# Kernel tuning notes

Measured on AMD Instinct MI355X. Metric: run time of the kernel, lower is better.

Reference implementation:

```python
import jax, jax.numpy as jnp
import numpy as np


def setup_inputs() -> dict:
    key = jax.random.key(0)
    k1, k2 = jax.random.split(key)
    N_ACTIVE = 262144
    C = 64            # nPlanes
    S = 64            # spatial_size per dim (3D)
    B = 8             # batch size
    features = jax.random.normal(k1, (N_ACTIVE, C), dtype=jnp.float32)
    # rule book: flat linear index of each active site into (b, z, y, x)
    idx = jax.random.randint(k2, (N_ACTIVE,), 0, B * S * S * S, dtype=jnp.int64)
    return {"features": features, "idx": idx, "spatial_size": S, "batch_size": B}


def reference(features, idx, spatial_size, batch_size):
    # Scatter sparse active-site features into dense grid.
    # features: [N, C], idx: [N] flat index over (b, z, y, x).
    N, C = features.shape
    S = spatial_size
    B = batch_size
    dense = jnp.zeros((B * S * S * S, C), dtype=features.dtype)
    # active sites in SparseConvNet are unique -> add == set, but add has a
    # well-defined gradient (pure gather) matching SparseToDense_updateGradInput
    dense = dense.at[idx].add(features)
    # [B, S, S, S, C] -> [B, C, S, S, S] (torch channels-first layout)
    dense = dense.reshape(B, S, S, S, C)
    return jnp.transpose(dense, (0, 4, 1, 2, 3))
```

## Files before the change

kernel.cpp:

```cpp
#include <hip/hip_runtime.h>


#define C_CH      64
#define LOG_C     6
#define LOG_S3    18
#define S3        (1 << LOG_S3)
#define NCELL     (8 * S3)
#define OUT_ELEMS (8LL * C_CH * S3)
#define TILE_S    256
#define CHUNK_C   16

typedef float v4f __attribute__((ext_vector_type(4)));

__global__ void build_lists_kernel(const int* __restrict__ idx,
                                   int* __restrict__ head,
                                   int* __restrict__ nxt, int n) {
    int i = blockIdx.x * blockDim.x + threadIdx.x;
    if (i < n) {
        int cell = idx[i];
        nxt[i] = atomicExch(&head[cell], i);
    }
}

__global__ void __launch_bounds__(256)
emit_tile_kernel(const float* __restrict__ feat,
                 const int* __restrict__ head,
                 const int* __restrict__ nxt,
                 float* __restrict__ out) {
    __shared__ float tile[CHUNK_C * TILE_S];

    const int b      = blockIdx.x >> 10;
    const int s_base = (blockIdx.x & 1023) << 8;
    const int t      = threadIdx.x;

    const int h = head[((size_t)b << LOG_S3) + s_base + t];

    const int lane = t & 63;
    const int wave = t >> 6;

    #pragma unroll 1
    for (int chunk = 0; chunk < C_CH / CHUNK_C; ++chunk) {
        v4f* t4 = (v4f*)tile;
        #pragma unroll
        for (int k = 0; k < 4; ++k)
            t4[t + 256 * k] = (v4f){0.f, 0.f, 0.f, 0.f};
        __syncthreads();

        int p = h;
        while (p >= 0) {
            const int pn = nxt[p];
            const v4f* fr = (const v4f*)(feat + ((size_t)p << LOG_C)
                                         + (chunk << 4));
            v4f f0 = fr[0], f1 = fr[1], f2 = fr[2], f3 = fr[3];
            float* col = tile + t;
            col[0*TILE_S]  += f0.x;  col[1*TILE_S]  += f0.y;
            col[2*TILE_S]  += f0.z;  col[3*TILE_S]  += f0.w;
            col[4*TILE_S]  += f1.x;  col[5*TILE_S]  += f1.y;
            col[6*TILE_S]  += f1.z;  col[7*TILE_S]  += f1.w;
            col[8*TILE_S]  += f2.x;  col[9*TILE_S]  += f2.y;
            col[10*TILE_S] += f2.z;  col[11*TILE_S] += f2.w;
            col[12*TILE_S] += f3.x;  col[13*TILE_S] += f3.y;
            col[14*TILE_S] += f3.z;  col[15*TILE_S] += f3.w;
            p = pn;
        }
        __syncthreads();

        #pragma unroll
        for (int r = 0; r < 4; ++r) {
            const int c = wave + (r << 2);
            v4f v = *(const v4f*)(tile + c * TILE_S + (lane << 2));
            const int c_glob = (b << LOG_C) + (chunk << 4) + c;
            __builtin_nontemporal_store(
                v, (v4f*)(out + (((size_t)c_glob) << LOG_S3)
                          + s_base + (lane << 2)));
        }
        __syncthreads();
    }
}

__global__ void zero_out_kernel(float4* __restrict__ out) {
    long long i = (long long)blockIdx.x * blockDim.x + threadIdx.x;
    out[i] = make_float4(0.f, 0.f, 0.f, 0.f);
}

__global__ void scatter_atomic_kernel(const float* __restrict__ feat,
                                      const int* __restrict__ idx,
                                      float* __restrict__ out, int n) {
    int i = blockIdx.x * blockDim.x + threadIdx.x;
    int nn = i >> LOG_C;
    int c  = i & (C_CH - 1);
    if (nn < n) {
        int cell = idx[nn];
        int b = cell >> LOG_S3;
        int s = cell & (S3 - 1);
        long long o = (((long long)((b << LOG_C) + c)) << LOG_S3) + s;
        atomicAdd(&out[o], feat[i]);
    }
}

extern "C" void kernel_launch(void* const* d_in, const int* in_sizes, int n_in,
                              void* d_out, int out_size, void* d_ws, size_t ws_size,
                              hipStream_t stream) {
    const float* feat = (const float*)d_in[0];
    const int*   idx  = (const int*)d_in[1];
    float*       out  = (float*)d_out;
    const int N = in_sizes[1];

    const size_t head_bytes = (size_t)NCELL * sizeof(int);
    const size_t next_bytes = (size_t)N * sizeof(int);

    if (ws_size >= head_bytes + next_bytes) {
        int* head = (int*)d_ws;
        int* nxt  = (int*)((char*)d_ws + head_bytes);

        build_lists_kernel<<<(N + 255) / 256, 256, 0, stream>>>(idx, head, nxt, N);
        emit_tile_kernel<<<NCELL / TILE_S, 256, 0, stream>>>(feat, head, nxt, out);
    } else {
        zero_out_kernel<<<(int)(OUT_ELEMS / 4 / 256), 256, 0, stream>>>((float4*)out);
        scatter_atomic_kernel<<<(N * C_CH) / 256, 256, 0, stream>>>(feat, idx, out, N);
    }
}
```

Before: 613.1 us.

## Replace LDS tile with per-thread register accumulators across 4 cells

Each thread now owns four consecutive cells and a 16-channel slice chosen by its wave, accumulating into registers instead of an LDS tile. This removes the per-chunk LDS zeroing, the read-modify-write shared memory traffic and three barriers per chunk, and it writes all output rows in one burst at the end. In exchange the linked-list walks for the four cells run serially within a thread, and register pressure rises.

Result: no change. 618.7 us (+0.9%).

```diff
diff --git a/kernel.cpp b/kernel.cpp
--- a/kernel.cpp
+++ b/kernel.cpp
@@ -8,7 +8,6 @@
 #define NCELL     (8 * S3)
 #define OUT_ELEMS (8LL * C_CH * S3)
 #define TILE_S    256
-#define CHUNK_C   16
 
 typedef float v4f __attribute__((ext_vector_type(4)));
 
@@ -22,59 +21,53 @@
     }
 }
 
-__global__ void __launch_bounds__(256)
-emit_tile_kernel(const float* __restrict__ feat,
-                 const int* __restrict__ head,
-                 const int* __restrict__ nxt,
-                 float* __restrict__ out) {
-    __shared__ float tile[CHUNK_C * TILE_S];
-
+__global__ void __launch_bounds__(256, 4)
+emit_reg_kernel(const float* __restrict__ feat,
+                const int* __restrict__ head,
+                const int* __restrict__ nxt,
+                float* __restrict__ out) {
     const int b      = blockIdx.x >> 10;
     const int s_base = (blockIdx.x & 1023) << 8;
     const int t      = threadIdx.x;
+    const int lane   = t & 63;
+    const int wave   = t >> 6;
 
-    const int h = head[((size_t)b << LOG_S3) + s_base + t];
+    const int4 h4 = *(const int4*)(head + ((size_t)b << LOG_S3)
+                                   + s_base + (lane << 2));
 
-    const int lane = t & 63;
-    const int wave = t >> 6;
+    v4f acc[16];
+    #pragma unroll
+    for (int c = 0; c < 16; ++c)
+        acc[c] = (v4f){0.f, 0.f, 0.f, 0.f};
 
-    #pragma unroll 1
-    for (int chunk = 0; chunk < C_CH / CHUNK_C; ++chunk) {
-        v4f* t4 = (v4f*)tile;
-        #pragma unroll
-        for (int k = 0; k < 4; ++k)
-            t4[t + 256 * k] = (v4f){0.f, 0.f, 0.f, 0.f};
-        __syncthreads();
+    const size_t chunk_off = (size_t)(wave << 4);
 
-        int p = h;
+    #pragma unroll
+    for (int j = 0; j < 4; ++j) {
+        int p = (j == 0) ? h4.x : (j == 1) ? h4.y : (j == 2) ? h4.z : h4.w;
         while (p >= 0) {
             const int pn = nxt[p];
             const v4f* fr = (const v4f*)(feat + ((size_t)p << LOG_C)
-                                         + (chunk << 4));
+                                         + chunk_off);
             v4f f0 = fr[0], f1 = fr[1], f2 = fr[2], f3 = fr[3];
-            float* col = tile + t;
-            col[0*TILE_S]  += f0.x;  col[1*TILE_S]  += f0.y;
-            col[2*TILE_S]  += f0.z;  col[3*TILE_S]  += f0.w;
-            col[4*TILE_S]  += f1.x;  col[5*TILE_S]  += f1.y;
-            col[6*TILE_S]  += f1.z;  col[7*TILE_S]  += f1.w;
-            col[8*TILE_S]  += f2.x;  col[9*TILE_S]  += f2.y;
-            col[10*TILE_S] += f2.z;  col[11*TILE_S] += f2.w;
-            col[12*TILE_S] += f3.x;  col[13*TILE_S] += f3.y;
-            col[14*TILE_S] += f3.z;  col[15*TILE_S] += f3.w;
+            #pragma unroll
+            for (int k = 0; k < 4; ++k) {
+                v4f f = (k == 0) ? f0 : (k == 1) ? f1 : (k == 2) ? f2 : f3;
+                acc[4*k + 0][j] += f.x;
+                acc[4*k + 1][j] += f.y;
+                acc[4*k + 2][j] += f.z;
+                acc[4*k + 3][j] += f.w;
+            }
             p = pn;
         }
-        __syncthreads();
+    }
 
-        #pragma unroll
-        for (int r = 0; r < 4; ++r) {
-            const int c = wave + (r << 2);
-            v4f v = *(const v4f*)(tile + c * TILE_S + (lane << 2));
-            const int c_glob = (b << LOG_C) + (chunk << 4) + c;
-            __builtin_nontemporal_store(
-                v, (v4f*)(out + (((size_t)c_glob) << LOG_S3)
-                          + s_base + (lane << 2)));
-        }
-        __syncthreads();
+    const int c_base = (b << LOG_C) + (wave << 4);
+    float* obase = out + ((size_t)c_base << LOG_S3) + s_base + (lane << 2);
+    #pragma unroll
+    for (int c = 0; c < 16; ++c) {
+        __builtin_nontemporal_store(
+            acc[c], (v4f*)(obase + ((size_t)c << LOG_S3)));
     }
 }
 
@@ -114,7 +107,7 @@
         int* nxt  = (int*)((char*)d_ws + head_bytes);
 
         build_lists_kernel<<<(N + 255) / 256, 256, 0, stream>>>(idx, head, nxt, N);
-        emit_tile_kernel<<<NCELL / TILE_S, 256, 0, stream>>>(feat, head, nxt, out);
+        emit_reg_kernel<<<NCELL / TILE_S, 256, 0, stream>>>(feat, head, nxt, out);
     } else {
         zero_out_kernel<<<(int)(OUT_ELEMS / 4 / 256), 256, 0, stream>>>((float4*)out);
         scatter_atomic_kernel<<<(N * C_CH) / 256, 256, 0, stream>>>(feat, idx, out, N);
```
